# Kernel optimization log

Hardware: AMD Instinct MI355X
Metric: run time of the kernel (lower is better)

The kernel has to match this reference:

```python
import jax, jax.numpy as jnp
import numpy as np

B, N, D = 8, 256, 128
LN_EPS = 1e-5


def setup_inputs() -> dict:
    key = jax.random.key(0)
    ks = jax.random.split(key, 12)
    s = 0.02
    return {
        "node_features": jax.random.normal(ks[0], (B, N, D), dtype=jnp.float32),
        "adjacency": jax.random.uniform(ks[1], (B, N, N), dtype=jnp.float32),
        "msg_w1": jax.random.normal(ks[2], (2 * D, D), dtype=jnp.float32) * s,
        "msg_b1": jnp.zeros((D,), jnp.float32),
        "msg_w2": jax.random.normal(ks[3], (D, D), dtype=jnp.float32) * s,
        "msg_b2": jnp.zeros((D,), jnp.float32),
        "upd_w1": jax.random.normal(ks[4], (2 * D, D), dtype=jnp.float32) * s,
        "upd_b1": jnp.zeros((D,), jnp.float32),
        "upd_w2": jax.random.normal(ks[5], (D, D), dtype=jnp.float32) * s,
        "upd_b2": jnp.zeros((D,), jnp.float32),
        "ln_g": jnp.ones((D,), jnp.float32),
        "ln_b": jnp.zeros((D,), jnp.float32),
    }


def reference(node_features, adjacency, msg_w1, msg_b1, msg_w2, msg_b2,
              upd_w1, upd_b1, upd_w2, upd_b2, ln_g, ln_b):
    d = node_features.shape[-1]
    n = node_features.shape[1]
    # Split the concat-then-matmul: cat(x_i, x_j) @ W1 == x_i @ W1[:d] + x_j @ W1[d:]
    hi = node_features @ msg_w1[:d]          # [B,N,D] (receiver i contribution)
    hj = node_features @ msg_w1[d:]          # [B,N,D] (sender j contribution)
    h = jax.nn.relu(hi[:, :, None, :] + hj[:, None, :, :] + msg_b1)  # [B,N,N,D]
    # Edge weights with the i==j pairs excluded (loop skips self-edges)
    a = adjacency * (1.0 - jnp.eye(n, dtype=adjacency.dtype))        # [B,N,N]
    # sum_j (h @ W2 + b2) * a_ij  ==  (sum_j h * a_ij) @ W2 + b2 * sum_j a_ij
    s = jnp.einsum('bijd,bij->bid', h, a)    # [B,N,D]
    agg = s @ msg_w2 + msg_b2 * jnp.sum(a, axis=-1, keepdims=True)   # [B,N,D]
    u = jnp.concatenate([node_features, agg], axis=-1)               # [B,N,2D]
    upd = jax.nn.relu(u @ upd_w1 + upd_b1) @ upd_w2 + upd_b2         # [B,N,D]
    res = node_features + upd
    mu = jnp.mean(res, axis=-1, keepdims=True)
    var = jnp.var(res, axis=-1, keepdims=True)
    return (res - mu) / jnp.sqrt(var + LN_EPS) * ln_g + ln_b
```

## Files before the change

### kernel.cpp

```cpp
#include <hip/hip_runtime.h>

#define BB 8
#define NN 256
#define DD 128
#define LN_EPS 1e-5f

__global__ __launch_bounds__(512) void k_proj(const float* __restrict__ x,
                                              const float* __restrict__ w1,
                                              const float* __restrict__ b1,
                                              float* __restrict__ hi,
                                              float* __restrict__ hjb) {
    __shared__ float xs[8][DD];
    __shared__ float part_a[4][8][DD];
    __shared__ float part_b[4][8][DD];
    const int row0 = blockIdx.x * 8;
    const int tid  = threadIdx.x;
    #pragma unroll
    for (int t = tid; t < 8 * DD; t += 512)
        xs[t >> 7][t & 127] = x[row0 * DD + t];
    __syncthreads();

    const int dp = tid & 127;
    const int kg = tid >> 7;
    const int kb = kg * 32;

    float acc_a[8] = {}, acc_b[8] = {};
    #pragma unroll
    for (int k4 = 0; k4 < 8; ++k4) {
        const int k0 = kb + k4 * 4;
        float wa[4], wb[4];
        #pragma unroll
        for (int q = 0; q < 4; ++q) {
            wa[q] = w1[(k0 + q) * DD + dp];
            wb[q] = w1[(DD + k0 + q) * DD + dp];
        }
        #pragma unroll
        for (int r = 0; r < 8; ++r) {
            const float4 xv = *(const float4*)&xs[r][k0];
            acc_a[r] = fmaf(xv.x, wa[0], acc_a[r]);
            acc_a[r] = fmaf(xv.y, wa[1], acc_a[r]);
            acc_a[r] = fmaf(xv.z, wa[2], acc_a[r]);
            acc_a[r] = fmaf(xv.w, wa[3], acc_a[r]);
            acc_b[r] = fmaf(xv.x, wb[0], acc_b[r]);
            acc_b[r] = fmaf(xv.y, wb[1], acc_b[r]);
            acc_b[r] = fmaf(xv.z, wb[2], acc_b[r]);
            acc_b[r] = fmaf(xv.w, wb[3], acc_b[r]);
        }
    }
    #pragma unroll
    for (int r = 0; r < 8; ++r) {
        part_a[kg][r][dp] = acc_a[r];
        part_b[kg][r][dp] = acc_b[r];
    }
    __syncthreads();
    #pragma unroll
    for (int m = 0; m < 2; ++m) {
        int idx = tid + m * 512;
        int r = idx >> 7, d = idx & 127;
        float sa = part_a[0][r][d] + part_a[1][r][d] + part_a[2][r][d] + part_a[3][r][d];
        float sb = part_b[0][r][d] + part_b[1][r][d] + part_b[2][r][d] + part_b[3][r][d];
        hi [(row0 + r) * DD + d] = sa;
        hjb[(row0 + r) * DD + d] = sb + b1[d];
    }
}

__global__ __launch_bounds__(512) void k_fused(const float* __restrict__ adj,
                                               const float* __restrict__ x,
                                               const float* __restrict__ hi,
                                               const float* __restrict__ hjb,
                                               const float* __restrict__ w2,
                                               const float* __restrict__ b2,
                                               const float* __restrict__ w3,
                                               const float* __restrict__ b3,
                                               const float* __restrict__ w4,
                                               const float* __restrict__ b4,
                                               const float* __restrict__ g,
                                               const float* __restrict__ bet,
                                               float* __restrict__ out) {
    __shared__ float smem[13320];
    float* const a_t    = smem + 8192;
    float* const xs     = smem + 10240;
    float* const ssp    = smem + 11264;
    float* const aggs   = smem + 12288;
    float* const u1s    = smem + 8192;
    float* const resS   = smem + 9216;
    float* const part   = smem;
    float* const asum_s = smem + 13312;

    const int bid = blockIdx.x;
    const int b   = bid >> 5;
    const int i0  = (bid & 31) * 8;
    const int tid = threadIdx.x;

    #pragma unroll
    for (int t = 0; t < 4; ++t) {
        int idx = tid + t * 512;
        int il = idx >> 8, j = idx & 255;
        int i_g = i0 + il;
        float av = adj[((size_t)b * NN + i_g) * NN + j];
        a_t[il * 256 + j] = (j == i_g) ? 0.f : av;
    }
    #pragma unroll
    for (int t = 0; t < 2; ++t) {
        int idx = tid + t * 512;
        xs[idx] = x[((size_t)b * NN + i0) * DD + idx];
    }
    __syncthreads();

    {
        int w = tid >> 6, l = tid & 63;
        float s = a_t[w * 256 + l] + a_t[w * 256 + l + 64]
                + a_t[w * 256 + l + 128] + a_t[w * 256 + l + 192];
        #pragma unroll
        for (int m = 32; m; m >>= 1) s += __shfl_xor(s, m);
        if (l == 0) asum_s[w] = s;
    }

    const int dq  = tid & 31;
    const int rg  = tid >> 5;
    const int row = rg & 7;
    const int jh  = rg >> 3;
    const float4 hi4 = *(const float4*)&hi[((size_t)b * NN + i0 + row) * DD + dq * 4];
    float4 acc = {0.f, 0.f, 0.f, 0.f};

    for (int jt = 0; jt < 4; ++jt) {
        __syncthreads();
        const float4* src = (const float4*)(hjb + ((size_t)b * NN + jt * 64) * DD);
        float4* dst = (float4*)smem;
        #pragma unroll
        for (int t = 0; t < 4; ++t) dst[tid + t * 512] = src[tid + t * 512];
        __syncthreads();
        const int jb = jh * 32;
        #pragma unroll 8
        for (int jj = 0; jj < 32; ++jj) {
            const int jl = jb + jj;
            const float4 hv = *(const float4*)&smem[jl * 128 + dq * 4];
            const float a = a_t[row * 256 + jt * 64 + jl];
            acc.x = fmaf(fmaxf(hi4.x + hv.x, 0.f), a, acc.x);
            acc.y = fmaf(fmaxf(hi4.y + hv.y, 0.f), a, acc.y);
            acc.z = fmaf(fmaxf(hi4.z + hv.z, 0.f), a, acc.z);
            acc.w = fmaf(fmaxf(hi4.w + hv.w, 0.f), a, acc.w);
        }
    }
    __syncthreads();
    *(float4*)&ssp[rg * 128 + dq * 4] = acc;
    __syncthreads();
    #pragma unroll
    for (int t = 0; t < 2; ++t) {
        int idx = tid + t * 512;
        int r = idx >> 7, d = idx & 127;
        ssp[r * 128 + d] += ssp[(r + 8) * 128 + d];
    }
    __syncthreads();

    const int dp = tid & 63;
    const int kg = tid >> 6;
    const int kb = kg * 16;

    {
        float wv0[16], wv1[16];
        #pragma unroll
        for (int k = 0; k < 16; ++k) {
            wv0[k] = w2[(kb + k) * DD + dp];
            wv1[k] = w2[(kb + k) * DD + dp + 64];
        }
        #pragma unroll
        for (int r = 0; r < 8; ++r) {
            float a0 = 0.f, a1 = 0.f;
            #pragma unroll
            for (int q = 0; q < 4; ++q) {
                const float4 sv = *(const float4*)&ssp[r * 128 + kb + q * 4];
                a0 = fmaf(sv.x, wv0[q*4+0], a0); a1 = fmaf(sv.x, wv1[q*4+0], a1);
                a0 = fmaf(sv.y, wv0[q*4+1], a0); a1 = fmaf(sv.y, wv1[q*4+1], a1);
                a0 = fmaf(sv.z, wv0[q*4+2], a0); a1 = fmaf(sv.z, wv1[q*4+2], a1);
                a0 = fmaf(sv.w, wv0[q*4+3], a0); a1 = fmaf(sv.w, wv1[q*4+3], a1);
            }
            part[kg * 1024 + r * 128 + dp]      = a0;
            part[kg * 1024 + r * 128 + dp + 64] = a1;
        }
    }
    __syncthreads();
    #pragma unroll
    for (int t = 0; t < 2; ++t) {
        int idx = tid + t * 512;
        int r = idx >> 7, d = idx & 127;
        float s = part[r * 128 + d];
        #pragma unroll
        for (int w = 1; w < 8; ++w) s += part[w * 1024 + r * 128 + d];
        aggs[r * 128 + d] = s + b2[d] * asum_s[r];
    }
    __syncthreads();

    {
        float wa0[16], wa1[16], wb0[16], wb1[16];
        #pragma unroll
        for (int k = 0; k < 16; ++k) {
            wa0[k] = w3[(kb + k) * DD + dp];
            wa1[k] = w3[(kb + k) * DD + dp + 64];
            wb0[k] = w3[(DD + kb + k) * DD + dp];
            wb1[k] = w3[(DD + kb + k) * DD + dp + 64];
        }
        #pragma unroll
        for (int r = 0; r < 8; ++r) {
            float a0 = 0.f, a1 = 0.f;
            #pragma unroll
            for (int q = 0; q < 4; ++q) {
                const float4 xv = *(const float4*)&xs[r * 128 + kb + q * 4];
                const float4 av = *(const float4*)&aggs[r * 128 + kb + q * 4];
                a0 = fmaf(xv.x, wa0[q*4+0], a0); a1 = fmaf(xv.x, wa1[q*4+0], a1);
                a0 = fmaf(xv.y, wa0[q*4+1], a0); a1 = fmaf(xv.y, wa1[q*4+1], a1);
                a0 = fmaf(xv.z, wa0[q*4+2], a0); a1 = fmaf(xv.z, wa1[q*4+2], a1);
                a0 = fmaf(xv.w, wa0[q*4+3], a0); a1 = fmaf(xv.w, wa1[q*4+3], a1);
                a0 = fmaf(av.x, wb0[q*4+0], a0); a1 = fmaf(av.x, wb1[q*4+0], a1);
                a0 = fmaf(av.y, wb0[q*4+1], a0); a1 = fmaf(av.y, wb1[q*4+1], a1);
                a0 = fmaf(av.z, wb0[q*4+2], a0); a1 = fmaf(av.z, wb1[q*4+2], a1);
                a0 = fmaf(av.w, wb0[q*4+3], a0); a1 = fmaf(av.w, wb1[q*4+3], a1);
            }
            part[kg * 1024 + r * 128 + dp]      = a0;
            part[kg * 1024 + r * 128 + dp + 64] = a1;
        }
    }
    __syncthreads();
    #pragma unroll
    for (int t = 0; t < 2; ++t) {
        int idx = tid + t * 512;
        int r = idx >> 7, d = idx & 127;
        float s = part[r * 128 + d];
        #pragma unroll
        for (int w = 1; w < 8; ++w) s += part[w * 1024 + r * 128 + d];
        u1s[r * 128 + d] = fmaxf(s + b3[d], 0.f);
    }
    __syncthreads();

    {
        float wv0[16], wv1[16];
        #pragma unroll
        for (int k = 0; k < 16; ++k) {
            wv0[k] = w4[(kb + k) * DD + dp];
            wv1[k] = w4[(kb + k) * DD + dp + 64];
        }
        #pragma unroll
        for (int r = 0; r < 8; ++r) {
            float a0 = 0.f, a1 = 0.f;
            #pragma unroll
            for (int q = 0; q < 4; ++q) {
                const float4 uv = *(const float4*)&u1s[r * 128 + kb + q * 4];
                a0 = fmaf(uv.x, wv0[q*4+0], a0); a1 = fmaf(uv.x, wv1[q*4+0], a1);
                a0 = fmaf(uv.y, wv0[q*4+1], a0); a1 = fmaf(uv.y, wv1[q*4+1], a1);
                a0 = fmaf(uv.z, wv0[q*4+2], a0); a1 = fmaf(uv.z, wv1[q*4+2], a1);
                a0 = fmaf(uv.w, wv0[q*4+3], a0); a1 = fmaf(uv.w, wv1[q*4+3], a1);
            }
            part[kg * 1024 + r * 128 + dp]      = a0;
            part[kg * 1024 + r * 128 + dp + 64] = a1;
        }
    }
    __syncthreads();
    #pragma unroll
    for (int t = 0; t < 2; ++t) {
        int idx = tid + t * 512;
        int r = idx >> 7, d = idx & 127;
        float s = part[r * 128 + d];
        #pragma unroll
        for (int w = 1; w < 8; ++w) s += part[w * 1024 + r * 128 + d];
        resS[r * 128 + d] = xs[r * 128 + d] + s + b4[d];
    }
    __syncthreads();

    {
        const int r = tid >> 6, l = tid & 63;
        const float2 v = *(const float2*)&resS[r * 128 + l * 2];
        float s1 = v.x + v.y;
        float s2 = v.x * v.x + v.y * v.y;
        #pragma unroll
        for (int m = 32; m; m >>= 1) {
            s1 += __shfl_xor(s1, m);
            s2 += __shfl_xor(s2, m);
        }
        const float mu = s1 * (1.f / DD);
        const float rs = rsqrtf(s2 * (1.f / DD) - mu * mu + LN_EPS);
        const int d = l * 2;
        const float2 gv = *(const float2*)&g[d];
        const float2 bv = *(const float2*)&bet[d];
        float2 o;
        o.x = (v.x - mu) * rs * gv.x + bv.x;
        o.y = (v.y - mu) * rs * gv.y + bv.y;
        *(float2*)&out[((size_t)b * NN + i0 + r) * DD + d] = o;
    }
}

extern "C" void kernel_launch(void* const* d_in, const int* in_sizes, int n_in,
                              void* d_out, int out_size, void* d_ws, size_t ws_size,
                              hipStream_t stream) {
    (void)in_sizes; (void)n_in; (void)out_size; (void)ws_size;
    const float* x      = (const float*)d_in[0];
    const float* adj    = (const float*)d_in[1];
    const float* msg_w1 = (const float*)d_in[2];
    const float* msg_b1 = (const float*)d_in[3];
    const float* msg_w2 = (const float*)d_in[4];
    const float* msg_b2 = (const float*)d_in[5];
    const float* upd_w1 = (const float*)d_in[6];
    const float* upd_b1 = (const float*)d_in[7];
    const float* upd_w2 = (const float*)d_in[8];
    const float* upd_b2 = (const float*)d_in[9];
    const float* ln_g   = (const float*)d_in[10];
    const float* ln_b   = (const float*)d_in[11];
    float* out = (float*)d_out;

    const size_t BND = (size_t)BB * NN * DD;
    float* ws  = (float*)d_ws;
    float* hi  = ws;
    float* hjb = ws + BND;

    k_proj<<<dim3(BB * NN / 8), dim3(512), 0, stream>>>(x, msg_w1, msg_b1, hi, hjb);
    k_fused<<<dim3(256), dim3(512), 0, stream>>>(adj, x, hi, hjb,
                                                 msg_w2, msg_b2,
                                                 upd_w1, upd_b1, upd_w2, upd_b2,
                                                 ln_g, ln_b, out);
}
```

Before: 28.77 us.

## Hoist x@upd_w1 into projection kernel and register-tile edge aggregation over rows

The x-half of the update MLP's first layer (x @ upd_w1[:D] + b1) now runs in the projection kernel and is written to a new workspace buffer, so the fused kernel only does the agg-half matmul. The edge aggregation loop no longer stages hjb tiles through shared memory. Each thread holds four receiver rows and streams hjb from global, reading adjacency from a transposed, padded shared layout, which reuses each loaded hjb value across four rows. The adjacency row sums are folded into the load loop. The trade-offs are an extra global write and read of the new intermediate, heavier register use in both kernels, and more synchronisation passes in the projection reduction.

```diff
diff --git a/kernel.cpp b/kernel.cpp
--- a/kernel.cpp
+++ b/kernel.cpp
@@ -8,59 +8,94 @@
 __global__ __launch_bounds__(512) void k_proj(const float* __restrict__ x,
                                               const float* __restrict__ w1,
                                               const float* __restrict__ b1,
+                                              const float* __restrict__ w3,
+                                              const float* __restrict__ b3,
                                               float* __restrict__ hi,
-                                              float* __restrict__ hjb) {
-    __shared__ float xs[8][DD];
-    __shared__ float part_a[4][8][DD];
-    __shared__ float part_b[4][8][DD];
+                                              float* __restrict__ hjb,
+                                              float* __restrict__ xw3) {
+    __shared__ float xs[8 * DD];
+    __shared__ float part[8 * 1024];
     const int row0 = blockIdx.x * 8;
     const int tid  = threadIdx.x;
     #pragma unroll
-    for (int t = tid; t < 8 * DD; t += 512)
-        xs[t >> 7][t & 127] = x[row0 * DD + t];
-    __syncthreads();
-
-    const int dp = tid & 127;
-    const int kg = tid >> 7;
-    const int kb = kg * 32;
-
-    float acc_a[8] = {}, acc_b[8] = {};
-    #pragma unroll
-    for (int k4 = 0; k4 < 8; ++k4) {
-        const int k0 = kb + k4 * 4;
-        float wa[4], wb[4];
+    for (int t = 0; t < 2; ++t) {
+        int idx = tid + t * 512;
+        xs[idx] = x[row0 * DD + idx];
+    }
+    __syncthreads();
+
+    const int dp2 = (tid & 63) * 2;
+    const int kg  = tid >> 6;
+    const int kb  = kg * 16;
+
+    float2 acc_a[8], acc_b[8], acc_c[8];
+    #pragma unroll
+    for (int r = 0; r < 8; ++r) {
+        acc_a[r] = make_float2(0.f, 0.f);
+        acc_b[r] = make_float2(0.f, 0.f);
+        acc_c[r] = make_float2(0.f, 0.f);
+    }
+
+    #pragma unroll
+    for (int q4 = 0; q4 < 4; ++q4) {
+        const int k0 = kb + q4 * 4;
+        float2 wa[4], wb[4], wc[4];
         #pragma unroll
         for (int q = 0; q < 4; ++q) {
-            wa[q] = w1[(k0 + q) * DD + dp];
-            wb[q] = w1[(DD + k0 + q) * DD + dp];
+            wa[q] = *(const float2*)&w1[(k0 + q) * DD + dp2];
+            wb[q] = *(const float2*)&w1[(DD + k0 + q) * DD + dp2];
+            wc[q] = *(const float2*)&w3[(k0 + q) * DD + dp2];
         }
         #pragma unroll
         for (int r = 0; r < 8; ++r) {
-            const float4 xv = *(const float4*)&xs[r][k0];
-            acc_a[r] = fmaf(xv.x, wa[0], acc_a[r]);
-            acc_a[r] = fmaf(xv.y, wa[1], acc_a[r]);
-            acc_a[r] = fmaf(xv.z, wa[2], acc_a[r]);
-            acc_a[r] = fmaf(xv.w, wa[3], acc_a[r]);
-            acc_b[r] = fmaf(xv.x, wb[0], acc_b[r]);
-            acc_b[r] = fmaf(xv.y, wb[1], acc_b[r]);
-            acc_b[r] = fmaf(xv.z, wb[2], acc_b[r]);
-            acc_b[r] = fmaf(xv.w, wb[3], acc_b[r]);
-        }
-    }
-    #pragma unroll
-    for (int r = 0; r < 8; ++r) {
-        part_a[kg][r][dp] = acc_a[r];
-        part_b[kg][r][dp] = acc_b[r];
-    }
-    __syncthreads();
-    #pragma unroll
-    for (int m = 0; m < 2; ++m) {
-        int idx = tid + m * 512;
-        int r = idx >> 7, d = idx & 127;
-        float sa = part_a[0][r][d] + part_a[1][r][d] + part_a[2][r][d] + part_a[3][r][d];
-        float sb = part_b[0][r][d] + part_b[1][r][d] + part_b[2][r][d] + part_b[3][r][d];
-        hi [(row0 + r) * DD + d] = sa;
-        hjb[(row0 + r) * DD + d] = sb + b1[d];
+            const float4 xv = *(const float4*)&xs[r * DD + k0];
+            const float xq[4] = {xv.x, xv.y, xv.z, xv.w};
+            #pragma unroll
+            for (int q = 0; q < 4; ++q) {
+                acc_a[r].x = fmaf(xq[q], wa[q].x, acc_a[r].x);
+                acc_a[r].y = fmaf(xq[q], wa[q].y, acc_a[r].y);
+                acc_b[r].x = fmaf(xq[q], wb[q].x, acc_b[r].x);
+                acc_b[r].y = fmaf(xq[q], wb[q].y, acc_b[r].y);
+                acc_c[r].x = fmaf(xq[q], wc[q].x, acc_c[r].x);
+                acc_c[r].y = fmaf(xq[q], wc[q].y, acc_c[r].y);
+            }
+        }
+    }
+
+    #pragma unroll
+    for (int r = 0; r < 8; ++r) *(float2*)&part[kg * 1024 + r * DD + dp2] = acc_a[r];
+    __syncthreads();
+    #pragma unroll
+    for (int m = 0; m < 2; ++m) {
+        int idx = tid + m * 512; int r = idx >> 7, d = idx & 127;
+        float s = 0.f;
+        #pragma unroll
+        for (int w = 0; w < 8; ++w) s += part[w * 1024 + r * DD + d];
+        hi[(row0 + r) * DD + d] = s;
+    }
+    __syncthreads();
+    #pragma unroll
+    for (int r = 0; r < 8; ++r) *(float2*)&part[kg * 1024 + r * DD + dp2] = acc_b[r];
+    __syncthreads();
+    #pragma unroll
+    for (int m = 0; m < 2; ++m) {
+        int idx = tid + m * 512; int r = idx >> 7, d = idx & 127;
+        float s = 0.f;
+        #pragma unroll
+        for (int w = 0; w < 8; ++w) s += part[w * 1024 + r * DD + d];
+        hjb[(row0 + r) * DD + d] = s + b1[d];
+    }
+    __syncthreads();
+    #pragma unroll
+    for (int r = 0; r < 8; ++r) *(float2*)&part[kg * 1024 + r * DD + dp2] = acc_c[r];
+    __syncthreads();
+    #pragma unroll
+    for (int m = 0; m < 2; ++m) {
+        int idx = tid + m * 512; int r = idx >> 7, d = idx & 127;
+        float s = 0.f;
+        #pragma unroll
+        for (int w = 0; w < 8; ++w) s += part[w * 1024 + r * DD + d];
+        xw3[(row0 + r) * DD + d] = s + b3[d];
     }
 }
 
@@ -68,24 +103,24 @@
                                                const float* __restrict__ x,
                                                const float* __restrict__ hi,
                                                const float* __restrict__ hjb,
+                                               const float* __restrict__ xw3,
                                                const float* __restrict__ w2,
                                                const float* __restrict__ b2,
                                                const float* __restrict__ w3,
-                                               const float* __restrict__ b3,
                                                const float* __restrict__ w4,
                                                const float* __restrict__ b4,
                                                const float* __restrict__ g,
                                                const float* __restrict__ bet,
                                                float* __restrict__ out) {
-    __shared__ float smem[13320];
-    float* const a_t    = smem + 8192;
-    float* const xs     = smem + 10240;
-    float* const ssp    = smem + 11264;
-    float* const aggs   = smem + 12288;
-    float* const u1s    = smem + 8192;
-    float* const resS   = smem + 9216;
-    float* const part   = smem;
-    float* const asum_s = smem + 13312;
+    __shared__ float smem[13352];
+    float* const part     = smem;
+    float* const a_tt     = smem + 8192;
+    float* const u1s      = smem + 8192;
+    float* const resS     = smem + 9216;
+    float* const ssp      = smem + 11264;
+    float* const aggs     = smem + 12288;
+    float* const asum_sub = smem + 13312;
+    float* const asum_s   = smem + 13344;
 
     const int bid = blockIdx.x;
     const int b   = bid >> 5;
@@ -96,60 +131,69 @@
     for (int t = 0; t < 4; ++t) {
         int idx = tid + t * 512;
         int il = idx >> 8, j = idx & 255;
-        int i_g = i0 + il;
-        float av = adj[((size_t)b * NN + i_g) * NN + j];
-        a_t[il * 256 + j] = (j == i_g) ? 0.f : av;
-    }
-    #pragma unroll
-    for (int t = 0; t < 2; ++t) {
-        int idx = tid + t * 512;
-        xs[idx] = x[((size_t)b * NN + i0) * DD + idx];
-    }
-    __syncthreads();
-
-    {
-        int w = tid >> 6, l = tid & 63;
-        float s = a_t[w * 256 + l] + a_t[w * 256 + l + 64]
-                + a_t[w * 256 + l + 128] + a_t[w * 256 + l + 192];
+        int ig = i0 + il;
+        float av = adj[((size_t)b * NN + ig) * NN + j];
+        av = (j == ig) ? 0.f : av;
+        a_tt[j * 12 + il] = av;
+        float s = av;
         #pragma unroll
         for (int m = 32; m; m >>= 1) s += __shfl_xor(s, m);
-        if (l == 0) asum_s[w] = s;
-    }
-
-    const int dq  = tid & 31;
-    const int rg  = tid >> 5;
-    const int row = rg & 7;
-    const int jh  = rg >> 3;
-    const float4 hi4 = *(const float4*)&hi[((size_t)b * NN + i0 + row) * DD + dq * 4];
-    float4 acc = {0.f, 0.f, 0.f, 0.f};
-
-    for (int jt = 0; jt < 4; ++jt) {
-        __syncthreads();
-        const float4* src = (const float4*)(hjb + ((size_t)b * NN + jt * 64) * DD);
-        float4* dst = (float4*)smem;
-        #pragma unroll
-        for (int t = 0; t < 4; ++t) dst[tid + t * 512] = src[tid + t * 512];
-        __syncthreads();
-        const int jb = jh * 32;
-        #pragma unroll 8
+        if ((tid & 63) == 0) asum_sub[il * 4 + ((tid & 255) >> 6)] = s;
+    }
+    __syncthreads();
+
+    {
+        const int dq = tid & 31;
+        const int rh = (tid >> 5) & 1;
+        const int js = tid >> 6;
+        const int r0 = rh * 4;
+        const float* hib = hi + ((size_t)b * NN + i0 + r0) * DD + dq * 4;
+        const float4 hi0 = *(const float4*)(hib);
+        const float4 hi1 = *(const float4*)(hib + DD);
+        const float4 hi2 = *(const float4*)(hib + 2 * DD);
+        const float4 hi3 = *(const float4*)(hib + 3 * DD);
+        float4 ac0 = {0,0,0,0}, ac1 = {0,0,0,0}, ac2 = {0,0,0,0}, ac3 = {0,0,0,0};
+        const float* hp = hjb + ((size_t)b * NN + js * 32) * DD + dq * 4;
+        const float* ap = a_tt + (js * 32) * 12 + r0;
+        #pragma unroll 4
         for (int jj = 0; jj < 32; ++jj) {
-            const int jl = jb + jj;
-            const float4 hv = *(const float4*)&smem[jl * 128 + dq * 4];
-            const float a = a_t[row * 256 + jt * 64 + jl];
-            acc.x = fmaf(fmaxf(hi4.x + hv.x, 0.f), a, acc.x);
-            acc.y = fmaf(fmaxf(hi4.y + hv.y, 0.f), a, acc.y);
-            acc.z = fmaf(fmaxf(hi4.z + hv.z, 0.f), a, acc.z);
-            acc.w = fmaf(fmaxf(hi4.w + hv.w, 0.f), a, acc.w);
-        }
-    }
-    __syncthreads();
-    *(float4*)&ssp[rg * 128 + dq * 4] = acc;
-    __syncthreads();
-    #pragma unroll
-    for (int t = 0; t < 2; ++t) {
-        int idx = tid + t * 512;
-        int r = idx >> 7, d = idx & 127;
-        ssp[r * 128 + d] += ssp[(r + 8) * 128 + d];
+            const float4 hv = *(const float4*)(hp + jj * DD);
+            const float4 a4 = *(const float4*)(ap + jj * 12);
+            ac0.x = fmaf(fmaxf(hi0.x + hv.x, 0.f), a4.x, ac0.x);
+            ac0.y = fmaf(fmaxf(hi0.y + hv.y, 0.f), a4.x, ac0.y);
+            ac0.z = fmaf(fmaxf(hi0.z + hv.z, 0.f), a4.x, ac0.z);
+            ac0.w = fmaf(fmaxf(hi0.w + hv.w, 0.f), a4.x, ac0.w);
+            ac1.x = fmaf(fmaxf(hi1.x + hv.x, 0.f), a4.y, ac1.x);
+            ac1.y = fmaf(fmaxf(hi1.y + hv.y, 0.f), a4.y, ac1.y);
+            ac1.z = fmaf(fmaxf(hi1.z + hv.z, 0.f), a4.y, ac1.z);
+            ac1.w = fmaf(fmaxf(hi1.w + hv.w, 0.f), a4.y, ac1.w);
+            ac2.x = fmaf(fmaxf(hi2.x + hv.x, 0.f), a4.z, ac2.x);
+            ac2.y = fmaf(fmaxf(hi2.y + hv.y, 0.f), a4.z, ac2.y);
+            ac2.z = fmaf(fmaxf(hi2.z + hv.z, 0.f), a4.z, ac2.z);
+            ac2.w = fmaf(fmaxf(hi2.w + hv.w, 0.f), a4.z, ac2.w);
+            ac3.x = fmaf(fmaxf(hi3.x + hv.x, 0.f), a4.w, ac3.x);
+            ac3.y = fmaf(fmaxf(hi3.y + hv.y, 0.f), a4.w, ac3.y);
+            ac3.z = fmaf(fmaxf(hi3.z + hv.z, 0.f), a4.w, ac3.z);
+            ac3.w = fmaf(fmaxf(hi3.w + hv.w, 0.f), a4.w, ac3.w);
+        }
+        float* pp = part + js * 1024 + r0 * DD + dq * 4;
+        *(float4*)(pp)          = ac0;
+        *(float4*)(pp + DD)     = ac1;
+        *(float4*)(pp + 2 * DD) = ac2;
+        *(float4*)(pp + 3 * DD) = ac3;
+    }
+    __syncthreads();
+
+    if (tid < 8)
+        asum_s[tid] = asum_sub[tid * 4] + asum_sub[tid * 4 + 1]
+                    + asum_sub[tid * 4 + 2] + asum_sub[tid * 4 + 3];
+    #pragma unroll
+    for (int m = 0; m < 2; ++m) {
+        int idx = tid + m * 512;
+        float s = 0.f;
+        #pragma unroll
+        for (int w = 0; w < 8; ++w) s += part[w * 1024 + idx];
+        ssp[idx] = s;
     }
     __syncthreads();
 
@@ -169,66 +213,58 @@
             float a0 = 0.f, a1 = 0.f;
             #pragma unroll
             for (int q = 0; q < 4; ++q) {
-                const float4 sv = *(const float4*)&ssp[r * 128 + kb + q * 4];
+                const float4 sv = *(const float4*)&ssp[r * DD + kb + q * 4];
                 a0 = fmaf(sv.x, wv0[q*4+0], a0); a1 = fmaf(sv.x, wv1[q*4+0], a1);
                 a0 = fmaf(sv.y, wv0[q*4+1], a0); a1 = fmaf(sv.y, wv1[q*4+1], a1);
                 a0 = fmaf(sv.z, wv0[q*4+2], a0); a1 = fmaf(sv.z, wv1[q*4+2], a1);
                 a0 = fmaf(sv.w, wv0[q*4+3], a0); a1 = fmaf(sv.w, wv1[q*4+3], a1);
             }
-            part[kg * 1024 + r * 128 + dp]      = a0;
-            part[kg * 1024 + r * 128 + dp + 64] = a1;
-        }
-    }
-    __syncthreads();
-    #pragma unroll
-    for (int t = 0; t < 2; ++t) {
-        int idx = tid + t * 512;
-        int r = idx >> 7, d = idx & 127;
-        float s = part[r * 128 + d];
-        #pragma unroll
-        for (int w = 1; w < 8; ++w) s += part[w * 1024 + r * 128 + d];
-        aggs[r * 128 + d] = s + b2[d] * asum_s[r];
-    }
-    __syncthreads();
-
-    {
-        float wa0[16], wa1[16], wb0[16], wb1[16];
+            part[kg * 1024 + r * DD + dp]      = a0;
+            part[kg * 1024 + r * DD + dp + 64] = a1;
+        }
+    }
+    __syncthreads();
+    #pragma unroll
+    for (int m = 0; m < 2; ++m) {
+        int idx = tid + m * 512; int r = idx >> 7, d = idx & 127;
+        float s = 0.f;
+        #pragma unroll
+        for (int w = 0; w < 8; ++w) s += part[w * 1024 + idx];
+        aggs[idx] = s + b2[d] * asum_s[r];
+    }
+    __syncthreads();
+
+    {
+        const float* w3b = w3 + DD * DD;
+        float wv0[16], wv1[16];
         #pragma unroll
         for (int k = 0; k < 16; ++k) {
-            wa0[k] = w3[(kb + k) * DD + dp];
-            wa1[k] = w3[(kb + k) * DD + dp + 64];
-            wb0[k] = w3[(DD + kb + k) * DD + dp];
-            wb1[k] = w3[(DD + kb + k) * DD + dp + 64];
+            wv0[k] = w3b[(kb + k) * DD + dp];
+            wv1[k] = w3b[(kb + k) * DD + dp + 64];
         }
         #pragma unroll
         for (int r = 0; r < 8; ++r) {
             float a0 = 0.f, a1 = 0.f;
             #pragma unroll
             for (int q = 0; q < 4; ++q) {
-                const float4 xv = *(const float4*)&xs[r * 128 + kb + q * 4];
-                const float4 av = *(const float4*)&aggs[r * 128 + kb + q * 4];
-                a0 = fmaf(xv.x, wa0[q*4+0], a0); a1 = fmaf(xv.x, wa1[q*4+0], a1);
-                a0 = fmaf(xv.y, wa0[q*4+1], a0); a1 = fmaf(xv.y, wa1[q*4+1], a1);
-                a0 = fmaf(xv.z, wa0[q*4+2], a0); a1 = fmaf(xv.z, wa1[q*4+2], a1);
-                a0 = fmaf(xv.w, wa0[q*4+3], a0); a1 = fmaf(xv.w, wa1[q*4+3], a1);
-                a0 = fmaf(av.x, wb0[q*4+0], a0); a1 = fmaf(av.x, wb1[q*4+0], a1);
-                a0 = fmaf(av.y, wb0[q*4+1], a0); a1 = fmaf(av.y, wb1[q*4+1], a1);
-                a0 = fmaf(av.z, wb0[q*4+2], a0); a1 = fmaf(av.z, wb1[q*4+2], a1);
-                a0 = fmaf(av.w, wb0[q*4+3], a0); a1 = fmaf(av.w, wb1[q*4+3], a1);
+                const float4 av = *(const float4*)&aggs[r * DD + kb + q * 4];
+                a0 = fmaf(av.x, wv0[q*4+0], a0); a1 = fmaf(av.x, wv1[q*4+0], a1);
+                a0 = fmaf(av.y, wv0[q*4+1], a0); a1 = fmaf(av.y, wv1[q*4+1], a1);
+                a0 = fmaf(av.z, wv0[q*4+2], a0); a1 = fmaf(av.z, wv1[q*4+2], a1);
+                a0 = fmaf(av.w, wv0[q*4+3], a0); a1 = fmaf(av.w, wv1[q*4+3], a1);
             }
-            part[kg * 1024 + r * 128 + dp]      = a0;
-            part[kg * 1024 + r * 128 + dp + 64] = a1;
-        }
-    }
-    __syncthreads();
-    #pragma unroll
-    for (int t = 0; t < 2; ++t) {
-        int idx = tid + t * 512;
-        int r = idx >> 7, d = idx & 127;
-        float s = part[r * 128 + d];
-        #pragma unroll
-        for (int w = 1; w < 8; ++w) s += part[w * 1024 + r * 128 + d];
-        u1s[r * 128 + d] = fmaxf(s + b3[d], 0.f);
+            part[kg * 1024 + r * DD + dp]      = a0;
+            part[kg * 1024 + r * DD + dp + 64] = a1;
+        }
+    }
+    __syncthreads();
+    #pragma unroll
+    for (int m = 0; m < 2; ++m) {
+        int idx = tid + m * 512;
+        float s = xw3[((size_t)b * NN + i0) * DD + idx];
+        #pragma unroll
+        for (int w = 0; w < 8; ++w) s += part[w * 1024 + idx];
+        u1s[idx] = fmaxf(s, 0.f);
     }
     __syncthreads();
 
@@ -244,31 +280,30 @@
             float a0 = 0.f, a1 = 0.f;
             #pragma unroll
             for (int q = 0; q < 4; ++q) {
-                const float4 uv = *(const float4*)&u1s[r * 128 + kb + q * 4];
+                const float4 uv = *(const float4*)&u1s[r * DD + kb + q * 4];
                 a0 = fmaf(uv.x, wv0[q*4+0], a0); a1 = fmaf(uv.x, wv1[q*4+0], a1);
                 a0 = fmaf(uv.y, wv0[q*4+1], a0); a1 = fmaf(uv.y, wv1[q*4+1], a1);
                 a0 = fmaf(uv.z, wv0[q*4+2], a0); a1 = fmaf(uv.z, wv1[q*4+2], a1);
                 a0 = fmaf(uv.w, wv0[q*4+3], a0); a1 = fmaf(uv.w, wv1[q*4+3], a1);
             }
-            part[kg * 1024 + r * 128 + dp]      = a0;
-            part[kg * 1024 + r * 128 + dp + 64] = a1;
-        }
-    }
-    __syncthreads();
-    #pragma unroll
-    for (int t = 0; t < 2; ++t) {
-        int idx = tid + t * 512;
-        int r = idx >> 7, d = idx & 127;
-        float s = part[r * 128 + d];
-        #pragma unroll
-        for (int w = 1; w < 8; ++w) s += part[w * 1024 + r * 128 + d];
-        resS[r * 128 + d] = xs[r * 128 + d] + s + b4[d];
+            part[kg * 1024 + r * DD + dp]      = a0;
+            part[kg * 1024 + r * DD + dp + 64] = a1;
+        }
+    }
+    __syncthreads();
+    #pragma unroll
+    for (int m = 0; m < 2; ++m) {
+        int idx = tid + m * 512; int d = idx & 127;
+        float s = x[((size_t)b * NN + i0) * DD + idx] + b4[d];
+        #pragma unroll
+        for (int w = 0; w < 8; ++w) s += part[w * 1024 + idx];
+        resS[idx] = s;
     }
     __syncthreads();
 
     {
         const int r = tid >> 6, l = tid & 63;
-        const float2 v = *(const float2*)&resS[r * 128 + l * 2];
+        const float2 v = *(const float2*)&resS[r * DD + l * 2];
         float s1 = v.x + v.y;
         float s2 = v.x * v.x + v.y * v.y;
         #pragma unroll
@@ -310,10 +345,13 @@
     float* ws  = (float*)d_ws;
     float* hi  = ws;
     float* hjb = ws + BND;
-
-    k_proj<<<dim3(BB * NN / 8), dim3(512), 0, stream>>>(x, msg_w1, msg_b1, hi, hjb);
-    k_fused<<<dim3(256), dim3(512), 0, stream>>>(adj, x, hi, hjb,
+    float* xw3 = ws + 2 * BND;
+
+    k_proj<<<dim3(BB * NN / 8), dim3(512), 0, stream>>>(x, msg_w1, msg_b1,
+                                                        upd_w1, upd_b1,
+                                                        hi, hjb, xw3);
+    k_fused<<<dim3(256), dim3(512), 0, stream>>>(adj, x, hi, hjb, xw3,
                                                  msg_w2, msg_b2,
-                                                 upd_w1, upd_b1, upd_w2, upd_b2,
+                                                 upd_w1, upd_w2, upd_b2,
                                                  ln_g, ln_b, out);
 }
```

Result: slower. 31.80 us (+10.5%).
